# Optimization experiments

Measured on AMD Instinct MI355X. Metric: run time of the kernel, lower is better.

The kernel has to match this reference:

```python
import jax, jax.numpy as jnp
import numpy as np
from jax import lax

NUM_TAGS = 9
HIDDEN = 768
BATCH = 64
SEQ = 512


def setup_inputs() -> dict:
    key = jax.random.key(0)
    ks = jax.random.split(key, 6)
    hidden = jax.random.normal(ks[0], (BATCH, SEQ, HIDDEN), dtype=jnp.float32)
    labels = jax.random.randint(ks[1], (BATCH, SEQ), 0, NUM_TAGS)  # all >= 0 -> full mask
    weight = jax.random.normal(ks[2], (NUM_TAGS, HIDDEN), dtype=jnp.float32) * 0.02
    bias = jnp.zeros((NUM_TAGS,), dtype=jnp.float32)
    start_transitions = jax.random.normal(ks[3], (NUM_TAGS,), dtype=jnp.float32) * 0.1
    end_transitions = jax.random.normal(ks[4], (NUM_TAGS,), dtype=jnp.float32) * 0.1
    transitions = jax.random.normal(ks[5], (NUM_TAGS, NUM_TAGS), dtype=jnp.float32) * 0.1
    return dict(hidden=hidden, labels=labels, weight=weight, bias=bias,
                start_transitions=start_transitions, end_transitions=end_transitions,
                transitions=transitions)


def _crf_log_likelihood(emissions, tags, mask, start_t, end_t, trans):
    """pytorch-crf log-likelihood, reduction='sum'.
    emissions [B,L,T] float, tags [B,L] int, mask [B,L] bool."""
    # --- numerator: score of the gold path ---
    tag0 = tags[:, 0]
    score0 = start_t[tag0] + jnp.take_along_axis(emissions[:, 0], tag0[:, None], axis=1)[:, 0]

    def num_step(carry, inp):
        score, prev = carry
        em, tg, m = inp  # em [B,T], tg [B], m [B]
        s = trans[prev, tg] + jnp.take_along_axis(em, tg[:, None], axis=1)[:, 0]
        score = score + jnp.where(m, s, jnp.zeros_like(s))
        prev = jnp.where(m, tg, prev)
        return (score, prev), None

    (num_score, last_tag), _ = lax.scan(
        num_step, (score0, tag0),
        (emissions[:, 1:].swapaxes(0, 1), tags[:, 1:].T, mask[:, 1:].T))
    numerator = num_score + end_t[last_tag]

    # --- denominator: forward algorithm (log-sum-exp recurrence) ---
    alpha0 = start_t[None, :] + emissions[:, 0]  # [B,T]

    def den_step(alpha, inp):
        em, m = inp  # em [B,T], m [B]
        nxt = jax.nn.logsumexp(alpha[:, :, None] + trans[None], axis=1) + em
        alpha = jnp.where(m[:, None], nxt, alpha)
        return alpha, None

    alpha, _ = lax.scan(den_step, alpha0,
                        (emissions[:, 1:].swapaxes(0, 1), mask[:, 1:].T))
    denominator = jax.nn.logsumexp(alpha + end_t[None, :], axis=1)

    return jnp.sum(numerator - denominator)


def _viterbi_decode(emissions, mask, start_t, end_t, trans):
    """Max-plus DP + backtrack. Returns padded [B,L] int32 best tag sequence."""
    B, L, T = emissions.shape
    score0 = start_t[None, :] + emissions[:, 0]  # [B,T]
    identity = jnp.arange(T, dtype=jnp.int32)[None, :]  # identity backpointer for masked steps

    def fwd_step(score, inp):
        em, m = inp  # em [B,T], m [B]
        br = score[:, :, None] + trans[None]  # [B,T_prev,T_cur]
        idx = jnp.argmax(br, axis=1).astype(jnp.int32)  # [B,T]
        nxt = jnp.max(br, axis=1) + em
        score = jnp.where(m[:, None], nxt, score)
        idx = jnp.where(m[:, None], idx, identity)
        return score, idx

    final, hist = lax.scan(fwd_step, score0,
                           (emissions[:, 1:].swapaxes(0, 1), mask[:, 1:].T))
    last_tag = jnp.argmax(final + end_t[None, :], axis=1).astype(jnp.int32)  # [B]

    def back_step(tag, idx):  # idx [B,T] backpointers for this position
        prev = jnp.take_along_axis(idx, tag[:, None], axis=1)[:, 0]
        return prev, tag

    first_tag, tags_rev = lax.scan(back_step, last_tag, hist, reverse=True)
    tags = jnp.concatenate([first_tag[None, :], tags_rev], axis=0).T  # [B,L]
    return tags * mask.astype(jnp.int32)


def reference(hidden, labels, weight, bias, start_transitions, end_transitions, transitions):
    mask_full = labels >= 0
    h = hidden[:, 1:-1, :]                       # drop [CLS]/[SEP] positions
    tags = labels[:, 1:-1] * mask_full[:, 1:-1]  # zero out padded labels
    mask = mask_full[:, 1:-1]
    # dropout is identity in eval mode
    emissions = jnp.einsum('blh,th->blt', h, weight) + bias  # [B,L,T]
    llh = _crf_log_likelihood(emissions, tags, mask,
                              start_transitions, end_transitions, transitions)
    tag_seqs = _viterbi_decode(emissions, mask,
                               start_transitions, end_transitions, transitions)
    return -llh, tag_seqs.astype(jnp.float32)
```

## Files before the change

### kernel.cpp

```cpp
#include <hip/hip_runtime.h>
#include <stdint.h>

#define NB 64
#define SEQL 512
#define L 510
#define T 9
#define H 768
#define EMS 12
#define LN2 0.6931471805599453f

__device__ __forceinline__ float rl(float v, int l) {
  return __uint_as_float(__builtin_amdgcn_readlane(__float_as_uint(v), l));
}

__global__ __launch_bounds__(256) void emis_chunk_kernel(
    const float* __restrict__ hidden, const float* __restrict__ weight,
    const float* __restrict__ bias, const float* __restrict__ trans,
    float* __restrict__ em, float* __restrict__ PdLn, float* __restrict__ Mv,
    float* __restrict__ out) {
  __shared__ float4 wl[T * 192];
  __shared__ __align__(16) float s_em[65][12];
  __shared__ __align__(16) float s_ee[65][12];
  const float4* w4 = (const float4*)weight;
  for (int k = threadIdx.x; k < T * 192; k += 256) wl[k] = w4[k];
  if (blockIdx.x == 0 && threadIdx.x == 0) out[0] = 0.f;
  __syncthreads();
  const int b = blockIdx.x >> 3;
  const int p = blockIdx.x & 7;
  const int row0 = p * 64;
  const int lane = threadIdx.x & 63;
  const int wv = threadIdx.x >> 6;
  const int npair = (wv == 0) ? 9 : 8;
#pragma unroll 1
  for (int pr = 0; pr < npair; ++pr) {
    const int i0 = (pr < 8) ? (wv * 16 + pr * 2) : 64;
    const int i1 = (pr < 8) ? (i0 + 1) : 64;
    const int r0 = row0 + i0, r1 = row0 + i1;
    const bool v0 = (r0 < L);
    const bool v1 = (r1 < L) && (pr < 8);
    const int c0 = v0 ? r0 : 0;
    const int c1 = (r1 < L) ? r1 : 0;
    const float4* h0 = (const float4*)(hidden + ((size_t)(b * SEQL + c0 + 1)) * H);
    const float4* h1 = (const float4*)(hidden + ((size_t)(b * SEQL + c1 + 1)) * H);
    float4 ha[3], hb[3];
#pragma unroll
    for (int k = 0; k < 3; ++k) { ha[k] = h0[lane + 64 * k]; hb[k] = h1[lane + 64 * k]; }
    float a0[T], a1[T];
#pragma unroll
    for (int t = 0; t < T; ++t) { a0[t] = 0.f; a1[t] = 0.f; }
#pragma unroll
    for (int t = 0; t < T; ++t) {
#pragma unroll
      for (int k = 0; k < 3; ++k) {
        float4 w = wl[t * 192 + lane + 64 * k];
        a0[t] = fmaf(ha[k].x, w.x, fmaf(ha[k].y, w.y, fmaf(ha[k].z, w.z, fmaf(ha[k].w, w.w, a0[t]))));
        a1[t] = fmaf(hb[k].x, w.x, fmaf(hb[k].y, w.y, fmaf(hb[k].z, w.z, fmaf(hb[k].w, w.w, a1[t]))));
      }
    }
#pragma unroll
    for (int off = 32; off; off >>= 1) {
#pragma unroll
      for (int t = 0; t < T; ++t) {
        a0[t] += __shfl_xor(a0[t], off);
        a1[t] += __shfl_xor(a1[t], off);
      }
    }
    if (lane < 2) {
      const bool vv = lane ? v1 : v0;
      const int ii = lane ? i1 : i0;
      if (vv) {
#pragma unroll
        for (int t = 0; t < T; ++t) {
          float v = (lane ? a1[t] : a0[t]) + bias[t];
          s_em[ii][t] = v;
          s_ee[ii][t] = __expf(v);
        }
      }
    }
  }
  __syncthreads();
  {
    const int nf4 = (p == 7) ? 186 : 192;
    if (threadIdx.x < nf4) {
      float4* dst = (float4*)(em + ((size_t)(b * L + row0)) * EMS);
      dst[threadIdx.x] = ((const float4*)s_em)[threadIdx.x];
    }
  }
  const int cb = wv & 1;
  const int sc_ = 2 * p + cb;
  const int task = b * 16 + sc_;
  const int nt = (sc_ == 15) ? 29 : 32;
  const int base = 1 + 32 * cb;
  const int i9 = (lane < 9) ? lane : 8;
  if (wv < 2) {
    float E[81];
#pragma unroll
    for (int k = 0; k < 81; ++k) E[k] = __expf(trans[k]);
    float R[9];
#pragma unroll
    for (int j = 0; j < 9; ++j) R[j] = E[i9 * 9 + j] * s_ee[base][j];
    int iexp = 0;
    for (int t = 1; t < nt; ++t) {
      float Rn[9];
#pragma unroll
      for (int j = 0; j < 9; ++j) {
        float a = R[0] * E[j];
#pragma unroll
        for (int k = 1; k < 9; ++k) a = fmaf(R[k], E[k * 9 + j], a);
        Rn[j] = a;
      }
#pragma unroll
      for (int j = 0; j < 9; ++j) R[j] = Rn[j] * s_ee[base + t][j];
      if ((t & 3) == 0) {
        float mx = R[0];
#pragma unroll
        for (int j = 1; j < 9; ++j) mx = fmaxf(mx, R[j]);
        int ex = (int)((__float_as_uint(mx) >> 23) & 0xff) - 127;
        iexp += ex;
        float sc = __uint_as_float((uint32_t)(127 - ex) << 23);
#pragma unroll
        for (int j = 0; j < 9; ++j) R[j] *= sc;
      }
    }
    if (lane < 9) {
      float ls = (float)iexp * LN2;
#pragma unroll
      for (int j = 0; j < 9; ++j)
        PdLn[(size_t)task * 81 + j * 9 + i9] = __logf(R[j]) + ls;
    }
  } else {
    float t_[81];
#pragma unroll
    for (int k = 0; k < 81; ++k) t_[k] = trans[k];
    float V[9];
#pragma unroll
    for (int j = 0; j < 9; ++j) V[j] = t_[i9 * 9 + j] + s_em[base][j];
    for (int t = 1; t < nt; ++t) {
      float Vn[9];
#pragma unroll
      for (int j = 0; j < 9; ++j) {
        float m = V[0] + t_[0 * 9 + j];
#pragma unroll
        for (int k = 1; k < 9; ++k) m = fmaxf(m, V[k] + t_[k * 9 + j]);
        Vn[j] = m + s_em[base + t][j];
      }
#pragma unroll
      for (int j = 0; j < 9; ++j) V[j] = Vn[j];
    }
    if (lane < 9) {
#pragma unroll
      for (int j = 0; j < 9; ++j)
        Mv[(size_t)task * 81 + j * 9 + i9] = V[j];
    }
  }
}

#define EADDR(l) ((l) * 12 + ((l) >> 5) * 4)
__global__ __launch_bounds__(64) void compose_path_kernel(
    const float* __restrict__ em, const int* __restrict__ labels,
    const float* __restrict__ PdLn, const float* __restrict__ Mv,
    const float* __restrict__ start_t, const float* __restrict__ end_t,
    const float* __restrict__ trans, float* __restrict__ out) {
  __shared__ float s_pd[16 * 81];
  __shared__ float s_mv[16 * 81];
  __shared__ float s_A[17 * 9];
  __shared__ float s_t[81];
  __shared__ int s_lab[L];
  __shared__ __align__(16) float s_e[510 * 12 + 64];
  __shared__ uint32_t s_bp[32][16][2];
  __shared__ int s_ch[16][2];
  const int b = blockIdx.x;
  const int lane = threadIdx.x;
  const float4* eg = (const float4*)(em + (size_t)b * L * EMS);
  for (int k = lane; k < 1530; k += 64) {
    const int l = k / 3, part = k - l * 3;
    *(float4*)&s_e[(size_t)EADDR(l) + part * 4] = eg[k];
  }
  for (int k = lane; k < 16 * 81; k += 64) {
    s_pd[k] = PdLn[(size_t)b * 16 * 81 + k];
    s_mv[k] = Mv[(size_t)b * 16 * 81 + k];
  }
  for (int k = lane; k < 81; k += 64) s_t[k] = trans[k];
  for (int k = lane; k < L; k += 64) s_lab[k] = labels[b * SEQL + 1 + k];
  __syncthreads();

  const int jj = lane < 9 ? lane : 8;

  float part_ = 0.f;
  for (int l = lane; l < L; l += 64) {
    int tg = s_lab[l];
    float e = s_e[EADDR(l) + tg];
    if (l == 0) part_ += start_t[tg] + e;
    else part_ += s_t[s_lab[l - 1] * 9 + tg] + e;
    if (l == L - 1) part_ += end_t[tg];
  }
#pragma unroll
  for (int off = 32; off; off >>= 1) part_ += __shfl_xor(part_, off);

  float D = start_t[jj] + s_e[jj];
  for (int u = 0; u < 16; ++u) {
    const float* col = &s_pd[u * 81 + jj * 9];
    float v0 = rl(D, 0) + col[0], v1 = rl(D, 1) + col[1], v2 = rl(D, 2) + col[2];
    float v3 = rl(D, 3) + col[3], v4 = rl(D, 4) + col[4], v5 = rl(D, 5) + col[5];
    float v6 = rl(D, 6) + col[6], v7 = rl(D, 7) + col[7], v8 = rl(D, 8) + col[8];
    float mx = fmaxf(fmaxf(fmaxf(fmaxf(v0, v1), fmaxf(v2, v3)),
                           fmaxf(fmaxf(v4, v5), fmaxf(v6, v7))), v8);
    float sum = __expf(v0 - mx) + __expf(v1 - mx) + __expf(v2 - mx) +
                __expf(v3 - mx) + __expf(v4 - mx) + __expf(v5 - mx) +
                __expf(v6 - mx) + __expf(v7 - mx) + __expf(v8 - mx);
    D = mx + __logf(sum);
  }
  float fe = D + end_t[jj];
  float w0 = rl(fe, 0), w1 = rl(fe, 1), w2 = rl(fe, 2), w3 = rl(fe, 3);
  float w4 = rl(fe, 4), w5 = rl(fe, 5), w6 = rl(fe, 6), w7 = rl(fe, 7), w8 = rl(fe, 8);
  float mx = fmaxf(fmaxf(fmaxf(fmaxf(w0, w1), fmaxf(w2, w3)),
                         fmaxf(fmaxf(w4, w5), fmaxf(w6, w7))), w8);
  float den = mx + __logf(__expf(w0 - mx) + __expf(w1 - mx) + __expf(w2 - mx) +
                          __expf(w3 - mx) + __expf(w4 - mx) + __expf(w5 - mx) +
                          __expf(w6 - mx) + __expf(w7 - mx) + __expf(w8 - mx));
  if (lane == 0) atomicAdd(out, den - part_);

  float A = start_t[jj] + s_e[jj];
  if (lane < 9) s_A[lane] = A;
  for (int u = 0; u < 16; ++u) {
    const float* col = &s_mv[u * 81 + jj * 9];
    float u0 = rl(A, 0) + col[0], u1 = rl(A, 1) + col[1], u2 = rl(A, 2) + col[2];
    float u3 = rl(A, 3) + col[3], u4 = rl(A, 4) + col[4], u5 = rl(A, 5) + col[5];
    float u6 = rl(A, 6) + col[6], u7 = rl(A, 7) + col[7], u8 = rl(A, 8) + col[8];
    A = fmaxf(fmaxf(fmaxf(fmaxf(u0, u1), fmaxf(u2, u3)),
                    fmaxf(fmaxf(u4, u5), fmaxf(u6, u7))), u8);
    if (lane < 9) s_A[(u + 1) * 9 + lane] = A;
  }
  float fv = A + end_t[jj];
  int j = 0;
  {
    float bv = rl(fv, 0);
#pragma unroll
    for (int i = 1; i < 9; ++i) { float v = rl(fv, i); if (v > bv) { bv = v; j = i; } }
  }
  for (int u = 15; u >= 0; --u) {
    float val = s_A[u * 9 + jj] + s_mv[u * 81 + j * 9 + jj];
    int ii = 0;
    float bb = rl(val, 0);
#pragma unroll
    for (int i = 1; i < 9; ++i) { float v = rl(val, i); if (v > bb) { bb = v; ii = i; } }
    if (lane == 0) { s_ch[u][0] = ii; s_ch[u][1] = j; }
    j = ii;
  }
  if (lane == 0) out[1 + (size_t)b * L] = (float)j;
  __syncthreads();

  if (lane < 16) {
    const int sch = lane;
    const int nt = (sch == 15) ? 29 : 32;
    const int lb = 32 * sch + 1;
    const int i0 = s_ch[sch][0];
    const int jF = s_ch[sch][1];
    float t_[81];
#pragma unroll
    for (int k = 0; k < 81; ++k) t_[k] = trans[k];
    float a[9];
    {
      const int ea = EADDR(lb);
#pragma unroll
      for (int jx = 0; jx < 9; ++jx) a[jx] = s_t[i0 * 9 + jx] + s_e[ea + jx];
    }
    for (int q = 1; q < nt; ++q) {
      const int ea = EADDR(lb + q);
      uint32_t pk0 = 0, pk1 = 0;
      float an[9];
#pragma unroll
      for (int jx = 0; jx < 9; ++jx) {
        float best = a[0] + t_[0 * 9 + jx];
        int bi = 0;
#pragma unroll
        for (int k = 1; k < 9; ++k) {
          float v = a[k] + t_[k * 9 + jx];
          if (v > best) { best = v; bi = k; }
        }
        an[jx] = best + s_e[ea + jx];
        if (jx < 8) pk0 |= ((uint32_t)bi) << (4 * jx);
        else pk1 = (uint32_t)bi;
      }
      s_bp[q][sch][0] = pk0;
      s_bp[q][sch][1] = pk1;
#pragma unroll
      for (int jx = 0; jx < 9; ++jx) a[jx] = an[jx];
    }
    int cur = jF;
    float* orow = out + 1 + (size_t)b * L + lb;
    for (int q = nt - 1; q >= 1; --q) {
      orow[q] = (float)cur;
      uint32_t w = s_bp[q][sch][cur >> 3];
      cur = (int)((w >> ((cur & 7) * 4)) & 15u);
    }
    orow[0] = (float)cur;
  }
}

extern "C" void kernel_launch(void* const* d_in, const int* in_sizes, int n_in,
                              void* d_out, int out_size, void* d_ws, size_t ws_size,
                              hipStream_t stream) {
  const float* hidden  = (const float*)d_in[0];
  const int*   labels  = (const int*)d_in[1];
  const float* weight  = (const float*)d_in[2];
  const float* bias    = (const float*)d_in[3];
  const float* start_t = (const float*)d_in[4];
  const float* end_t   = (const float*)d_in[5];
  const float* trans   = (const float*)d_in[6];
  float* out = (float*)d_out;

  float* em   = (float*)d_ws;
  float* PdLn = em + (size_t)NB * L * EMS;
  float* Mv   = PdLn + (size_t)1024 * 81;

  emis_chunk_kernel<<<512, 256, 0, stream>>>(hidden, weight, bias, trans,
                                             em, PdLn, Mv, out);
  compose_path_kernel<<<NB, 64, 0, stream>>>(em, labels, PdLn, Mv,
                                             start_t, end_t, trans, out);
}
```

Before: 242.1 us.

## Record Viterbi backpointers in chunk kernel and parallelize compose stage

The chunk kernel's max-plus pass now records packed per-start-tag backpointers for every chunk step, and it computes the gold-path score terms directly from shared emissions. The compose kernel therefore no longer reloads the full emission tensor or reruns a second Viterbi over each chunk; it only backtracks using the stored pointers. It also runs the forward log-sum-exp and the Viterbi composition on separate wavefronts in parallel. In exchange the first kernel does extra argmax bookkeeping and writes a larger backpointer buffer (9 start tags × 32 steps per chunk).

```diff
diff --git a/kernel.cpp b/kernel.cpp
--- a/kernel.cpp
+++ b/kernel.cpp
@@ -6,7 +6,6 @@
 #define L 510
 #define T 9
 #define H 768
-#define EMS 12
 #define LN2 0.6931471805599453f
 
 __device__ __forceinline__ float rl(float v, int l) {
@@ -16,8 +15,10 @@
 __global__ __launch_bounds__(256) void emis_chunk_kernel(
     const float* __restrict__ hidden, const float* __restrict__ weight,
     const float* __restrict__ bias, const float* __restrict__ trans,
-    float* __restrict__ em, float* __restrict__ PdLn, float* __restrict__ Mv,
-    float* __restrict__ out) {
+    const float* __restrict__ start_t, const float* __restrict__ end_t,
+    const int* __restrict__ labels, float* __restrict__ sel,
+    float* __restrict__ em0, float* __restrict__ PdLn, float* __restrict__ Mv,
+    unsigned long long* __restrict__ Bp, float* __restrict__ out) {
   __shared__ float4 wl[T * 192];
   __shared__ __align__(16) float s_em[65][12];
   __shared__ __align__(16) float s_ee[65][12];
@@ -79,13 +80,20 @@
     }
   }
   __syncthreads();
-  {
-    const int nf4 = (p == 7) ? 186 : 192;
-    if (threadIdx.x < nf4) {
-      float4* dst = (float4*)(em + ((size_t)(b * L + row0)) * EMS);
-      dst[threadIdx.x] = ((const float4*)s_em)[threadIdx.x];
-    }
-  }
+  if (threadIdx.x < 64) {
+    const int r = threadIdx.x;
+    const int l = row0 + r;
+    if (l < L) {
+      const int tg = labels[b * SEQL + 1 + l];
+      const float e = s_em[r][tg];
+      float term;
+      if (l == 0) term = start_t[tg] + e;
+      else term = trans[labels[b * SEQL + l] * 9 + tg] + e;
+      sel[b * 512 + l] = term;
+      if (l == L - 1) sel[b * 512 + 510] = end_t[tg];
+    }
+  }
+  if (p == 0 && threadIdx.x < 12) em0[b * 12 + threadIdx.x] = s_em[0][threadIdx.x];
   const int cb = wv & 1;
   const int sc_ = 2 * p + cb;
   const int task = b * 16 + sc_;
@@ -136,14 +144,24 @@
 #pragma unroll
     for (int j = 0; j < 9; ++j) V[j] = t_[i9 * 9 + j] + s_em[base][j];
     for (int t = 1; t < nt; ++t) {
+      uint32_t lo = 0, hi = 0;
       float Vn[9];
 #pragma unroll
       for (int j = 0; j < 9; ++j) {
-        float m = V[0] + t_[0 * 9 + j];
-#pragma unroll
-        for (int k = 1; k < 9; ++k) m = fmaxf(m, V[k] + t_[k * 9 + j]);
-        Vn[j] = m + s_em[base + t][j];
-      }
+        float best = V[0] + t_[0 * 9 + j];
+        int bi = 0;
+#pragma unroll
+        for (int k = 1; k < 9; ++k) {
+          float v = V[k] + t_[k * 9 + j];
+          if (v > best) { best = v; bi = k; }
+        }
+        Vn[j] = best + s_em[base + t][j];
+        if (j < 8) lo |= ((uint32_t)bi) << (4 * j);
+        else hi = (uint32_t)bi;
+      }
+      if (lane < 9)
+        Bp[(size_t)task * 288 + t * 9 + i9] =
+            (unsigned long long)lo | ((unsigned long long)hi << 32);
 #pragma unroll
       for (int j = 0; j < 9; ++j) V[j] = Vn[j];
     }
@@ -155,144 +173,107 @@
   }
 }
 
-#define EADDR(l) ((l) * 12 + ((l) >> 5) * 4)
-__global__ __launch_bounds__(64) void compose_path_kernel(
-    const float* __restrict__ em, const int* __restrict__ labels,
+__global__ __launch_bounds__(256) void compose_kernel(
+    const float* __restrict__ sel, const float* __restrict__ em0,
     const float* __restrict__ PdLn, const float* __restrict__ Mv,
+    const unsigned long long* __restrict__ Bp,
     const float* __restrict__ start_t, const float* __restrict__ end_t,
-    const float* __restrict__ trans, float* __restrict__ out) {
-  __shared__ float s_pd[16 * 81];
-  __shared__ float s_mv[16 * 81];
+    float* __restrict__ out) {
+  __shared__ __align__(16) float s_pd[16 * 81];
+  __shared__ __align__(16) float s_mv[16 * 81];
+  __shared__ __align__(16) unsigned long long s_bp[16 * 290];
   __shared__ float s_A[17 * 9];
-  __shared__ float s_t[81];
-  __shared__ int s_lab[L];
-  __shared__ __align__(16) float s_e[510 * 12 + 64];
-  __shared__ uint32_t s_bp[32][16][2];
   __shared__ int s_ch[16][2];
   const int b = blockIdx.x;
-  const int lane = threadIdx.x;
-  const float4* eg = (const float4*)(em + (size_t)b * L * EMS);
-  for (int k = lane; k < 1530; k += 64) {
-    const int l = k / 3, part = k - l * 3;
-    *(float4*)&s_e[(size_t)EADDR(l) + part * 4] = eg[k];
-  }
-  for (int k = lane; k < 16 * 81; k += 64) {
-    s_pd[k] = PdLn[(size_t)b * 16 * 81 + k];
-    s_mv[k] = Mv[(size_t)b * 16 * 81 + k];
-  }
-  for (int k = lane; k < 81; k += 64) s_t[k] = trans[k];
-  for (int k = lane; k < L; k += 64) s_lab[k] = labels[b * SEQL + 1 + k];
+  const int tid = threadIdx.x;
+  {
+    const float4* pdg = (const float4*)(PdLn + (size_t)b * 1296);
+    const float4* mvg = (const float4*)(Mv + (size_t)b * 1296);
+    for (int k = tid; k < 324; k += 256) {
+      ((float4*)s_pd)[k] = pdg[k];
+      ((float4*)s_mv)[k] = mvg[k];
+    }
+    const float4* bpg = (const float4*)(Bp + (size_t)b * 4608);
+    for (int k = tid; k < 2304; k += 256) {
+      const int s = k / 144, r = k - s * 144;
+      ((float4*)&s_bp[s * 290])[r] = bpg[k];
+    }
+  }
   __syncthreads();
-
+  const int wv = tid >> 6;
+  const int lane = tid & 63;
   const int jj = lane < 9 ? lane : 8;
 
-  float part_ = 0.f;
-  for (int l = lane; l < L; l += 64) {
-    int tg = s_lab[l];
-    float e = s_e[EADDR(l) + tg];
-    if (l == 0) part_ += start_t[tg] + e;
-    else part_ += s_t[s_lab[l - 1] * 9 + tg] + e;
-    if (l == L - 1) part_ += end_t[tg];
-  }
-#pragma unroll
-  for (int off = 32; off; off >>= 1) part_ += __shfl_xor(part_, off);
-
-  float D = start_t[jj] + s_e[jj];
-  for (int u = 0; u < 16; ++u) {
-    const float* col = &s_pd[u * 81 + jj * 9];
-    float v0 = rl(D, 0) + col[0], v1 = rl(D, 1) + col[1], v2 = rl(D, 2) + col[2];
-    float v3 = rl(D, 3) + col[3], v4 = rl(D, 4) + col[4], v5 = rl(D, 5) + col[5];
-    float v6 = rl(D, 6) + col[6], v7 = rl(D, 7) + col[7], v8 = rl(D, 8) + col[8];
-    float mx = fmaxf(fmaxf(fmaxf(fmaxf(v0, v1), fmaxf(v2, v3)),
-                           fmaxf(fmaxf(v4, v5), fmaxf(v6, v7))), v8);
-    float sum = __expf(v0 - mx) + __expf(v1 - mx) + __expf(v2 - mx) +
-                __expf(v3 - mx) + __expf(v4 - mx) + __expf(v5 - mx) +
-                __expf(v6 - mx) + __expf(v7 - mx) + __expf(v8 - mx);
-    D = mx + __logf(sum);
-  }
-  float fe = D + end_t[jj];
-  float w0 = rl(fe, 0), w1 = rl(fe, 1), w2 = rl(fe, 2), w3 = rl(fe, 3);
-  float w4 = rl(fe, 4), w5 = rl(fe, 5), w6 = rl(fe, 6), w7 = rl(fe, 7), w8 = rl(fe, 8);
-  float mx = fmaxf(fmaxf(fmaxf(fmaxf(w0, w1), fmaxf(w2, w3)),
-                         fmaxf(fmaxf(w4, w5), fmaxf(w6, w7))), w8);
-  float den = mx + __logf(__expf(w0 - mx) + __expf(w1 - mx) + __expf(w2 - mx) +
-                          __expf(w3 - mx) + __expf(w4 - mx) + __expf(w5 - mx) +
-                          __expf(w6 - mx) + __expf(w7 - mx) + __expf(w8 - mx));
-  if (lane == 0) atomicAdd(out, den - part_);
-
-  float A = start_t[jj] + s_e[jj];
-  if (lane < 9) s_A[lane] = A;
-  for (int u = 0; u < 16; ++u) {
-    const float* col = &s_mv[u * 81 + jj * 9];
-    float u0 = rl(A, 0) + col[0], u1 = rl(A, 1) + col[1], u2 = rl(A, 2) + col[2];
-    float u3 = rl(A, 3) + col[3], u4 = rl(A, 4) + col[4], u5 = rl(A, 5) + col[5];
-    float u6 = rl(A, 6) + col[6], u7 = rl(A, 7) + col[7], u8 = rl(A, 8) + col[8];
-    A = fmaxf(fmaxf(fmaxf(fmaxf(u0, u1), fmaxf(u2, u3)),
-                    fmaxf(fmaxf(u4, u5), fmaxf(u6, u7))), u8);
-    if (lane < 9) s_A[(u + 1) * 9 + lane] = A;
-  }
-  float fv = A + end_t[jj];
-  int j = 0;
-  {
-    float bv = rl(fv, 0);
-#pragma unroll
-    for (int i = 1; i < 9; ++i) { float v = rl(fv, i); if (v > bv) { bv = v; j = i; } }
-  }
-  for (int u = 15; u >= 0; --u) {
-    float val = s_A[u * 9 + jj] + s_mv[u * 81 + j * 9 + jj];
-    int ii = 0;
-    float bb = rl(val, 0);
-#pragma unroll
-    for (int i = 1; i < 9; ++i) { float v = rl(val, i); if (v > bb) { bb = v; ii = i; } }
-    if (lane == 0) { s_ch[u][0] = ii; s_ch[u][1] = j; }
-    j = ii;
-  }
-  if (lane == 0) out[1 + (size_t)b * L] = (float)j;
+  if (wv == 0) {
+    float part_ = 0.f;
+    for (int l = lane; l < L; l += 64) part_ += sel[b * 512 + l];
+    if (lane == 61) part_ += sel[b * 512 + 510];
+#pragma unroll
+    for (int off = 32; off; off >>= 1) part_ += __shfl_xor(part_, off);
+    float D = start_t[jj] + em0[b * 12 + jj];
+    for (int u = 0; u < 16; ++u) {
+      const float* col = &s_pd[u * 81 + jj * 9];
+      float v0 = rl(D, 0) + col[0], v1 = rl(D, 1) + col[1], v2 = rl(D, 2) + col[2];
+      float v3 = rl(D, 3) + col[3], v4 = rl(D, 4) + col[4], v5 = rl(D, 5) + col[5];
+      float v6 = rl(D, 6) + col[6], v7 = rl(D, 7) + col[7], v8 = rl(D, 8) + col[8];
+      float mx = fmaxf(fmaxf(fmaxf(fmaxf(v0, v1), fmaxf(v2, v3)),
+                             fmaxf(fmaxf(v4, v5), fmaxf(v6, v7))), v8);
+      float sum = __expf(v0 - mx) + __expf(v1 - mx) + __expf(v2 - mx) +
+                  __expf(v3 - mx) + __expf(v4 - mx) + __expf(v5 - mx) +
+                  __expf(v6 - mx) + __expf(v7 - mx) + __expf(v8 - mx);
+      D = mx + __logf(sum);
+    }
+    float fe = D + end_t[jj];
+    float w0 = rl(fe, 0), w1 = rl(fe, 1), w2 = rl(fe, 2), w3 = rl(fe, 3);
+    float w4 = rl(fe, 4), w5 = rl(fe, 5), w6 = rl(fe, 6), w7 = rl(fe, 7), w8 = rl(fe, 8);
+    float mx = fmaxf(fmaxf(fmaxf(fmaxf(w0, w1), fmaxf(w2, w3)),
+                           fmaxf(fmaxf(w4, w5), fmaxf(w6, w7))), w8);
+    float den = mx + __logf(__expf(w0 - mx) + __expf(w1 - mx) + __expf(w2 - mx) +
+                            __expf(w3 - mx) + __expf(w4 - mx) + __expf(w5 - mx) +
+                            __expf(w6 - mx) + __expf(w7 - mx) + __expf(w8 - mx));
+    if (lane == 0) atomicAdd(out, den - part_);
+  } else if (wv == 1) {
+    float A = start_t[jj] + em0[b * 12 + jj];
+    if (lane < 9) s_A[lane] = A;
+    for (int u = 0; u < 16; ++u) {
+      const float* col = &s_mv[u * 81 + jj * 9];
+      float u0 = rl(A, 0) + col[0], u1 = rl(A, 1) + col[1], u2 = rl(A, 2) + col[2];
+      float u3 = rl(A, 3) + col[3], u4 = rl(A, 4) + col[4], u5 = rl(A, 5) + col[5];
+      float u6 = rl(A, 6) + col[6], u7 = rl(A, 7) + col[7], u8 = rl(A, 8) + col[8];
+      A = fmaxf(fmaxf(fmaxf(fmaxf(u0, u1), fmaxf(u2, u3)),
+                      fmaxf(fmaxf(u4, u5), fmaxf(u6, u7))), u8);
+      if (lane < 9) s_A[(u + 1) * 9 + lane] = A;
+    }
+    float fv = A + end_t[jj];
+    int j = 0;
+    {
+      float bv = rl(fv, 0);
+#pragma unroll
+      for (int i = 1; i < 9; ++i) { float v = rl(fv, i); if (v > bv) { bv = v; j = i; } }
+    }
+    for (int u = 15; u >= 0; --u) {
+      float val = s_A[u * 9 + jj] + s_mv[u * 81 + j * 9 + jj];
+      int ii = 0;
+      float bb = rl(val, 0);
+#pragma unroll
+      for (int i = 1; i < 9; ++i) { float v = rl(val, i); if (v > bb) { bb = v; ii = i; } }
+      if (lane == 0) { s_ch[u][0] = ii; s_ch[u][1] = j; }
+      j = ii;
+    }
+    if (lane == 0) out[1 + (size_t)b * L] = (float)j;
+  }
   __syncthreads();
-
-  if (lane < 16) {
-    const int sch = lane;
-    const int nt = (sch == 15) ? 29 : 32;
-    const int lb = 32 * sch + 1;
-    const int i0 = s_ch[sch][0];
-    const int jF = s_ch[sch][1];
-    float t_[81];
-#pragma unroll
-    for (int k = 0; k < 81; ++k) t_[k] = trans[k];
-    float a[9];
-    {
-      const int ea = EADDR(lb);
-#pragma unroll
-      for (int jx = 0; jx < 9; ++jx) a[jx] = s_t[i0 * 9 + jx] + s_e[ea + jx];
-    }
-    for (int q = 1; q < nt; ++q) {
-      const int ea = EADDR(lb + q);
-      uint32_t pk0 = 0, pk1 = 0;
-      float an[9];
-#pragma unroll
-      for (int jx = 0; jx < 9; ++jx) {
-        float best = a[0] + t_[0 * 9 + jx];
-        int bi = 0;
-#pragma unroll
-        for (int k = 1; k < 9; ++k) {
-          float v = a[k] + t_[k * 9 + jx];
-          if (v > best) { best = v; bi = k; }
-        }
-        an[jx] = best + s_e[ea + jx];
-        if (jx < 8) pk0 |= ((uint32_t)bi) << (4 * jx);
-        else pk1 = (uint32_t)bi;
-      }
-      s_bp[q][sch][0] = pk0;
-      s_bp[q][sch][1] = pk1;
-#pragma unroll
-      for (int jx = 0; jx < 9; ++jx) a[jx] = an[jx];
-    }
-    int cur = jF;
+  if (wv == 2 && lane < 16) {
+    const int s = lane;
+    const int nt = (s == 15) ? 29 : 32;
+    const int lb = 32 * s + 1;
+    const int i0 = s_ch[s][0];
+    int cur = s_ch[s][1];
     float* orow = out + 1 + (size_t)b * L + lb;
     for (int q = nt - 1; q >= 1; --q) {
       orow[q] = (float)cur;
-      uint32_t w = s_bp[q][sch][cur >> 3];
-      cur = (int)((w >> ((cur & 7) * 4)) & 15u);
+      unsigned long long w = s_bp[s * 290 + q * 9 + i0];
+      cur = (int)((w >> (4 * cur)) & 15ULL);
     }
     orow[0] = (float)cur;
   }
@@ -310,12 +291,15 @@
   const float* trans   = (const float*)d_in[6];
   float* out = (float*)d_out;
 
-  float* em   = (float*)d_ws;
-  float* PdLn = em + (size_t)NB * L * EMS;
+  unsigned long long* Bp = (unsigned long long*)d_ws;
+  float* sel  = (float*)(Bp + (size_t)1024 * 288);
+  float* em0  = sel + (size_t)64 * 512;
+  float* PdLn = em0 + 768;
   float* Mv   = PdLn + (size_t)1024 * 81;
 
   emis_chunk_kernel<<<512, 256, 0, stream>>>(hidden, weight, bias, trans,
-                                             em, PdLn, Mv, out);
-  compose_path_kernel<<<NB, 64, 0, stream>>>(em, labels, PdLn, Mv,
-                                             start_t, end_t, trans, out);
+                                             start_t, end_t, labels,
+                                             sel, em0, PdLn, Mv, Bp, out);
+  compose_kernel<<<NB, 256, 0, stream>>>(sel, em0, PdLn, Mv, Bp,
+                                         start_t, end_t, out);
 }
```

New measurement: 242.0 us. No clear change (-0.0%).
